# Optimization experiments

Measured on AMD Instinct MI355X. Metric: run time of the kernel, lower is better.

## Reference

```python
import jax, jax.numpy as jnp
import numpy as np

WIDTH = 64
HEIGHT = 64
FEAT = 128
LAT = 64
NUM_SLOTS = 7


def pixel_coords(img_size):
    g = jnp.linspace(-1.0, 1.0, img_size)
    g1, g2 = jnp.meshgrid(g, g, indexing='ij')  # matches torch.meshgrid default
    return jnp.stack([g1, g2], axis=0)[None]  # (1, 2, S, S)


def clamp_pg(x, lo, hi):
    # clamp that preserves gradients (straight-through)
    return x + jax.lax.stop_gradient(jnp.clip(x, lo, hi) - x)


def setup_inputs() -> dict:
    key = jax.random.key(0)
    k0, k1, k2, k3 = jax.random.split(key, 4)
    bs = 64
    x = jax.random.normal(k0, (bs, FEAT, WIDTH, HEIGHT), jnp.float32)
    rand_pixel = jax.random.uniform(k1, (bs, 1, WIDTH, HEIGHT), jnp.float32)
    conv_w = jax.random.normal(k2, (LAT, FEAT), jnp.float32) / np.sqrt(FEAT)
    conv_b = jax.random.normal(k3, (LAT,), jnp.float32) * 0.01
    gate = jnp.asarray(0.5, jnp.float32)  # ScalarGate parameter (nonzero so c_f is non-degenerate)
    # laplacian kernel: sigma_init = 1 / (sqrt(num_slots) * log 2)
    log_sigma = jnp.asarray(np.log(1.0 / (np.sqrt(NUM_SLOTS) * np.log(2.0))), jnp.float32)
    return {'x': x, 'rand_pixel': rand_pixel, 'conv_w': conv_w, 'conv_b': conv_b,
            'gate': gate, 'log_sigma': log_sigma, 'num_cl_steps': 6}


def _forward(x, rand_pixel, conv_w, conv_b, gate, log_sigma, num_cl_steps):
    bs = x.shape[0]
    # SemiConv: gated 1x1 conv + fixed uv coordinate channels
    out = gate * (jnp.einsum('of,bfhw->bohw', conv_w, x) + conv_b[None, :, None, None])
    uv = jnp.concatenate([jnp.zeros((1, LAT - 2, WIDTH, HEIGHT), out.dtype),
                          pixel_coords(WIDTH).astype(out.dtype)], axis=1)
    c_f = out + uv                      # (bs, LAT, W, H)
    delta = out[:, -2:]                 # (bs, 2, W, H)
    sigma = jnp.exp(log_sigma)
    c_flat = c_f.reshape(bs, LAT, -1)   # (bs, LAT, W*H)
    b_idx = jnp.arange(bs)
    log_s0 = jnp.zeros((bs, 1, WIDTH, HEIGHT), c_f.dtype)

    def step(log_s, _):
        # interpolate-to-same-size is identity -> scope = exp(log_s)
        probs = (rand_pixel * jnp.exp(log_s)).reshape(bs, -1)
        idx = jnp.argmax(probs, axis=1)                 # (bs,)
        seed = c_flat[b_idx, :, idx]                    # (bs, LAT)
        diff = c_f - seed[:, :, None, None]
        dist = jnp.sqrt(clamp_pg((diff ** 2).sum(1), 1e-10, 1e10))  # euclidian (laplacian kernel)
        alpha = jnp.exp(-dist / sigma)[:, None]         # (bs, 1, W, H)
        alpha = clamp_pg(alpha, 0.01, 0.99)
        log_m = log_s + jnp.log(alpha)
        new_log_s = log_s + jnp.log1p(-alpha)
        return new_log_s, (log_m, new_log_s, seed)

    log_s_final, (log_m_steps, log_s_steps, seeds) = jax.lax.scan(
        step, log_s0, None, length=num_cl_steps)
    # log_m_k has num_cl_steps masks plus the final scope appended
    log_m_k = jnp.concatenate([log_m_steps, log_s_final[None]], axis=0)
    log_s_k = jnp.concatenate([log_s0[None], log_s_steps], axis=0)
    return log_m_k, log_s_k, c_f, delta, seeds


def reference(x, rand_pixel, conv_w, conv_b, gate, log_sigma, num_cl_steps):
    return _forward(x, rand_pixel, conv_w, conv_b, gate, log_sigma, num_cl_steps)
```

## Files before the change

kernel.cpp:

```cpp
#include <hip/hip_runtime.h>
#include <hip/hip_bf16.h>

#define NPIX 4096
#define FEAT 128
#define LAT 64
#define BS 64
#define NSTEPS 6

#define OFF_LOGM  0u
#define OFF_LOGS  1835008u
#define OFF_CF    3670016u
#define OFF_DELTA 20447232u
#define OFF_SEEDS 20971520u

typedef float f32x4 __attribute__((ext_vector_type(4)));
typedef short s16x8 __attribute__((ext_vector_type(8)));

__device__ __forceinline__ void amax_comb(float& bv, int& bi, float v, int i) {
    if (v > bv || (v == bv && i < bi)) { bv = v; bi = i; }
}

__device__ __forceinline__ short f2bf_rne(float r) {
    __hip_bfloat16 h = __float2bfloat16(r);
    return __builtin_bit_cast(short, h);
}

__device__ __forceinline__ void split2(float v, short& hi, short& lo) {
    unsigned u = __builtin_bit_cast(unsigned, v);
    hi = (short)(u >> 16);
    float hf = __builtin_bit_cast(float, u & 0xFFFF0000u);
    lo = f2bf_rne(v - hf);
}

__device__ __forceinline__ void transpose4(float4& v, int b) {
    float4 w;
    w.x = __shfl_xor(v.x, 1, 64); w.y = __shfl_xor(v.y, 1, 64);
    w.z = __shfl_xor(v.z, 1, 64); w.w = __shfl_xor(v.w, 1, 64);
    float4 u;
    if ((b & 1) == 0) u = make_float4(v.x, w.x, v.z, w.z);
    else              u = make_float4(w.y, v.y, w.w, v.w);
    float4 w2;
    w2.x = __shfl_xor(u.x, 2, 64); w2.y = __shfl_xor(u.y, 2, 64);
    w2.z = __shfl_xor(u.z, 2, 64); w2.w = __shfl_xor(u.w, 2, 64);
    if ((b & 2) == 0) v = make_float4(u.x, u.y, w2.x, w2.y);
    else              v = make_float4(w2.z, w2.w, u.z, u.w);
}

__global__ void prep_w(const float* __restrict__ w, const float* __restrict__ gate_p,
                       short* __restrict__ gwh, short* __restrict__ gwl)
{
    int i = blockIdx.x * 256 + threadIdx.x;
    float v = gate_p[0] * w[i];
    short h, l; split2(v, h, l);
    gwh[i] = h; gwl[i] = l;
}

__global__ __launch_bounds__(512, 4) void conv_mfma(
    const float* __restrict__ x, const float* __restrict__ rand_pixel,
    const float* __restrict__ bias, const float* __restrict__ gate_p,
    float* __restrict__ out,
    float* __restrict__ pval, int* __restrict__ pidx, int* __restrict__ cnt,
    const short* __restrict__ gwh, const short* __restrict__ gwl)
{
    __shared__ __align__(16) short Xhi[256][40];
    __shared__ __align__(16) short Xlo[256][40];
    __shared__ __align__(16) short Whi[64][132];
    __shared__ __align__(16) short Wlo[64][132];
    __shared__ float sbias[64];

    const int tid  = threadIdx.x;
    const int b    = blockIdx.x >> 4;
    const int tile = blockIdx.x & 15;
    const int p0   = tile * 256;
    const int lane = tid & 63;
    const int wv   = tid >> 6;
    const int l15  = lane & 15;
    const int lg   = lane >> 4;
    const int oh   = wv >> 2;
    const int pxq  = wv & 3;

    const int q  = tid >> 2;
    const int j  = tid & 3;
    const int P  = (q & 63) * 4;
    const int g0 = q >> 6;

    if (tile == 0 && tid < 8) cnt[b * 8 + tid] = 0;
    if (tid < 64) sbias[tid] = gate_p[0] * bias[tid];

    {
        const int o = tid >> 3, c = (tid & 7) * 16;
        *(s16x8*)&Whi[o][c]     = *(const s16x8*)&gwh[o * 128 + c];
        *(s16x8*)&Whi[o][c + 8] = *(const s16x8*)&gwh[o * 128 + c + 8];
        *(s16x8*)&Wlo[o][c]     = *(const s16x8*)&gwl[o * 128 + c];
        *(s16x8*)&Wlo[o][c + 8] = *(const s16x8*)&gwl[o * 128 + c + 8];
    }

    const float* xb = x + (size_t)b * FEAT * NPIX + p0;
    float4 v[4];
    #pragma unroll
    for (int i = 0; i < 4; ++i) {
        int g = g0 + 2 * i;
        v[i] = *(const float4*)(xb + (size_t)(g * 4 + j) * NPIX + P);
    }
    #pragma unroll
    for (int i = 0; i < 4; ++i) {
        int g = g0 + 2 * i;
        float4 t = v[i]; transpose4(t, j);
        short h0, l0, h1, l1, h2, l2, h3, l3;
        split2(t.x, h0, l0); split2(t.y, h1, l1);
        split2(t.z, h2, l2); split2(t.w, h3, l3);
        *(short4*)&Xhi[P + j][g * 4] = make_short4(h0, h1, h2, h3);
        *(short4*)&Xlo[P + j][g * 4] = make_short4(l0, l1, l2, l3);
    }
    __syncthreads();

    f32x4 acc[2][4];
    #pragma unroll
    for (int og2 = 0; og2 < 2; ++og2)
        #pragma unroll
        for (int pg = 0; pg < 4; ++pg)
            acc[og2][pg] = (f32x4){0.f, 0.f, 0.f, 0.f};

    #pragma unroll
    for (int kc = 0; kc < 4; ++kc) {
        if (kc < 3) {
            #pragma unroll
            for (int i = 0; i < 4; ++i) {
                int g = g0 + 2 * i;
                v[i] = *(const float4*)(xb + (size_t)((kc + 1) * 32 + g * 4 + j) * NPIX + P);
            }
        }

        s16x8 Ah[2], Al[2];
        #pragma unroll
        for (int og2 = 0; og2 < 2; ++og2) {
            int o = oh * 32 + og2 * 16 + l15;
            Ah[og2] = *(const s16x8*)&Whi[o][kc * 32 + lg * 8];
            Al[og2] = *(const s16x8*)&Wlo[o][kc * 32 + lg * 8];
        }

        #pragma unroll
        for (int pg = 0; pg < 4; ++pg) {
            int pxl = pxq * 64 + pg * 16 + l15;
            s16x8 Bh = *(const s16x8*)&Xhi[pxl][lg * 8];
            s16x8 Bl = *(const s16x8*)&Xlo[pxl][lg * 8];
            #pragma unroll
            for (int og2 = 0; og2 < 2; ++og2) {
                acc[og2][pg] = __builtin_amdgcn_mfma_f32_16x16x32_bf16(Ah[og2], Bh, acc[og2][pg], 0, 0, 0);
                acc[og2][pg] = __builtin_amdgcn_mfma_f32_16x16x32_bf16(Ah[og2], Bl, acc[og2][pg], 0, 0, 0);
                acc[og2][pg] = __builtin_amdgcn_mfma_f32_16x16x32_bf16(Al[og2], Bh, acc[og2][pg], 0, 0, 0);
            }
        }

        if (kc < 3) {
            __syncthreads();
            #pragma unroll
            for (int i = 0; i < 4; ++i) {
                int g = g0 + 2 * i;
                float4 t = v[i]; transpose4(t, j);
                short h0, l0, h1, l1, h2, l2, h3, l3;
                split2(t.x, h0, l0); split2(t.y, h1, l1);
                split2(t.z, h2, l2); split2(t.w, h3, l3);
                *(short4*)&Xhi[P + j][g * 4] = make_short4(h0, h1, h2, h3);
                *(short4*)&Xlo[P + j][g * 4] = make_short4(l0, l1, l2, l3);
            }
            __syncthreads();
        }
    }

    float* cf = out + OFF_CF + (size_t)b * LAT * NPIX;
    #pragma unroll
    for (int og2 = 0; og2 < 2; ++og2) {
        #pragma unroll
        for (int pg = 0; pg < 4; ++pg) {
            #pragma unroll
            for (int r = 0; r < 4; ++r) {
                int o = oh * 32 + og2 * 16 + lg * 4 + r;
                int p = p0 + pxq * 64 + pg * 16 + l15;
                float vv = acc[og2][pg][r] + sbias[o];
                if (o == 62) {
                    out[OFF_DELTA + ((size_t)b * 2 + 0) * NPIX + p] = vv;
                    vv += (float)(-1.0 + 2.0 * (double)(p >> 6) / 63.0);
                } else if (o == 63) {
                    out[OFF_DELTA + ((size_t)b * 2 + 1) * NPIX + p] = vv;
                    vv += (float)(-1.0 + 2.0 * (double)(p & 63) / 63.0);
                }
                cf[(size_t)o * NPIX + p] = vv;
            }
        }
    }

    if (wv == 0) {
        *(float4*)(out + OFF_LOGS + (size_t)b * NPIX + p0 + lane * 4) =
            make_float4(0.f, 0.f, 0.f, 0.f);
        float4 rv = *(const float4*)(rand_pixel + (size_t)b * NPIX + p0 + lane * 4);
        int pb = p0 + lane * 4;
        float bv = rv.x; int bi = pb;
        if (rv.y > bv) { bv = rv.y; bi = pb + 1; }
        if (rv.z > bv) { bv = rv.z; bi = pb + 2; }
        if (rv.w > bv) { bv = rv.w; bi = pb + 3; }
        #pragma unroll
        for (int off = 32; off > 0; off >>= 1) {
            float ov = __shfl_down(bv, off, 64);
            int   oi = __shfl_down(bi, off, 64);
            amax_comb(bv, bi, ov, oi);
        }
        if (lane == 0) { pval[blockIdx.x] = bv; pidx[blockIdx.x] = bi; }
    }
}

#define REP16(OP) OP(0) OP(1) OP(2) OP(3) OP(4) OP(5) OP(6) OP(7) \
                  OP(8) OP(9) OP(10) OP(11) OP(12) OP(13) OP(14) OP(15)

__global__ __launch_bounds__(1024, 4) void steps_fused(
    const float* __restrict__ rand_pixel, const float* __restrict__ log_sigma_p,
    float* __restrict__ out, float* pv, int* pi, int* cnt)
{
    __shared__ float s_mv[16];
    __shared__ int   s_mi[16];
    __shared__ __align__(16) float s_seed[LAT];
    __shared__ float s_rv[16];
    __shared__ int   s_ri[16];

    const int tid  = threadIdx.x;
    const int b    = blockIdx.x & 63;
    const int tile = blockIdx.x >> 6;
    const int p    = tile * 1024 + tid;

    const float* cfb = out + OFF_CF + (size_t)b * LAT * NPIX;

#define AG_DECL(i) float ag##i##_0, ag##i##_1, ag##i##_2, ag##i##_3;
    REP16(AG_DECL)
#define AG_PARK(i) { \
    float v0 = cfb[(size_t)(4*i+0)*NPIX + p]; \
    float v1 = cfb[(size_t)(4*i+1)*NPIX + p]; \
    float v2 = cfb[(size_t)(4*i+2)*NPIX + p]; \
    float v3 = cfb[(size_t)(4*i+3)*NPIX + p]; \
    asm volatile("v_accvgpr_write_b32 %0, %1" : "=a"(ag##i##_0) : "v"(v0)); \
    asm volatile("v_accvgpr_write_b32 %0, %1" : "=a"(ag##i##_1) : "v"(v1)); \
    asm volatile("v_accvgpr_write_b32 %0, %1" : "=a"(ag##i##_2) : "v"(v2)); \
    asm volatile("v_accvgpr_write_b32 %0, %1" : "=a"(ag##i##_3) : "v"(v3)); }
    REP16(AG_PARK)

    const float rp    = rand_pixel[(size_t)b * NPIX + p];
    const float sigma = expf(log_sigma_p[0]);
    float ls = 0.f;

    #pragma unroll 1
    for (int s = 0; s < NSTEPS; ++s) {
        if (s > 0) {
            if (tid == 0) {
                while (__hip_atomic_load(&cnt[b * 8 + s], __ATOMIC_ACQUIRE,
                                         __HIP_MEMORY_SCOPE_AGENT) < 4)
                    __builtin_amdgcn_s_sleep(2);
            }
            __syncthreads();
        }
        const int nmerge = (s == 0) ? 16 : 4;
        if (tid < nmerge) {
            s_mv[tid] = __hip_atomic_load(&pv[(s * BS + b) * 16 + tid],
                                          __ATOMIC_RELAXED, __HIP_MEMORY_SCOPE_AGENT);
            s_mi[tid] = __hip_atomic_load(&pi[(s * BS + b) * 16 + tid],
                                          __ATOMIC_RELAXED, __HIP_MEMORY_SCOPE_AGENT);
        }
        __syncthreads();

        float bv = -1.0f; int bi = 0;
        for (int k = 0; k < nmerge; ++k) amax_comb(bv, bi, s_mv[k], s_mi[k]);

        if (tid < LAT) s_seed[tid] = cfb[(size_t)tid * NPIX + bi];
        __syncthreads();
        if (tile == 0 && tid < LAT)
            out[OFF_SEEDS + ((size_t)s * BS + b) * LAT + tid] = s_seed[tid];

        float d2 = 0.f;
#define AG_DIFF(i) { \
        float c0, c1, c2, c3; \
        asm volatile("v_accvgpr_read_b32 %0, %1" : "=v"(c0) : "a"(ag##i##_0)); \
        asm volatile("v_accvgpr_read_b32 %0, %1" : "=v"(c1) : "a"(ag##i##_1)); \
        asm volatile("v_accvgpr_read_b32 %0, %1" : "=v"(c2) : "a"(ag##i##_2)); \
        asm volatile("v_accvgpr_read_b32 %0, %1" : "=v"(c3) : "a"(ag##i##_3)); \
        float e0 = c0 - s_seed[4*i+0]; d2 = fmaf(e0, e0, d2); \
        float e1 = c1 - s_seed[4*i+1]; d2 = fmaf(e1, e1, d2); \
        float e2 = c2 - s_seed[4*i+2]; d2 = fmaf(e2, e2, d2); \
        float e3 = c3 - s_seed[4*i+3]; d2 = fmaf(e3, e3, d2); }
        REP16(AG_DIFF)

        float dist  = sqrtf(fminf(fmaxf(d2, 1e-10f), 1e10f));
        float alpha = expf(-dist / sigma);
        alpha = fminf(fmaxf(alpha, 0.01f), 0.99f);
        float lm  = ls + logf(alpha);
        float lsn = ls + log1pf(-alpha);

        out[OFF_LOGM + ((size_t)s * BS + b) * NPIX + p]       = lm;
        out[OFF_LOGS + ((size_t)(s + 1) * BS + b) * NPIX + p] = lsn;
        ls = lsn;

        if (s == NSTEPS - 1) {
            out[OFF_LOGM + ((size_t)NSTEPS * BS + b) * NPIX + p] = lsn;
        } else {
            float prob = rp * expf(lsn);
            int   idx  = p;
            #pragma unroll
            for (int off = 32; off > 0; off >>= 1) {
                float ov = __shfl_down(prob, off, 64);
                int   oi = __shfl_down(idx, off, 64);
                amax_comb(prob, idx, ov, oi);
            }
            int lane = tid & 63, wid = tid >> 6;
            if (lane == 0) { s_rv[wid] = prob; s_ri[wid] = idx; }
            __syncthreads();
            if (tid == 0) {
                float fb = s_rv[0]; int fi = s_ri[0];
                #pragma unroll
                for (int k = 1; k < 16; ++k) amax_comb(fb, fi, s_rv[k], s_ri[k]);
                __hip_atomic_store(&pv[((s + 1) * BS + b) * 16 + tile], fb,
                                   __ATOMIC_RELAXED, __HIP_MEMORY_SCOPE_AGENT);
                __hip_atomic_store(&pi[((s + 1) * BS + b) * 16 + tile], fi,
                                   __ATOMIC_RELAXED, __HIP_MEMORY_SCOPE_AGENT);
                __hip_atomic_fetch_add(&cnt[b * 8 + s + 1], 1,
                                       __ATOMIC_RELEASE, __HIP_MEMORY_SCOPE_AGENT);
            }
        }
    }
}

__global__ __launch_bounds__(1024, 4) void step_kernel(
    const float* __restrict__ rand_pixel, const float* __restrict__ log_sigma_p,
    float* __restrict__ out, float* pv, int* pi, int step)
{
    __shared__ float s_mv[16];
    __shared__ int   s_mi[16];
    __shared__ __align__(16) float s_seed[LAT];
    __shared__ float s_rv[16];
    __shared__ int   s_ri[16];

    const int tid  = threadIdx.x;
    const int b    = blockIdx.x & 63;
    const int tile = blockIdx.x >> 6;
    const int p    = tile * 1024 + tid;

    const float* cfb = out + OFF_CF + (size_t)b * LAT * NPIX;

    const int nmerge = (step == 0) ? 16 : 4;
    if (tid < nmerge) { s_mv[tid] = pv[(step * BS + b) * 16 + tid];
                        s_mi[tid] = pi[(step * BS + b) * 16 + tid]; }
    __syncthreads();
    float bv = -1.0f; int bi = 0;
    for (int k = 0; k < nmerge; ++k) amax_comb(bv, bi, s_mv[k], s_mi[k]);

    if (tid < LAT) s_seed[tid] = cfb[(size_t)tid * NPIX + bi];
    __syncthreads();
    if (tile == 0 && tid < LAT)
        out[OFF_SEEDS + ((size_t)step * BS + b) * LAT + tid] = s_seed[tid];

    float d2 = 0.f;
    #pragma unroll
    for (int c = 0; c < LAT; ++c) {
        float d = cfb[(size_t)c * NPIX + p] - s_seed[c];
        d2 = fmaf(d, d, d2);
    }
    float dist  = sqrtf(fminf(fmaxf(d2, 1e-10f), 1e10f));
    float sigma = expf(log_sigma_p[0]);
    float alpha = expf(-dist / sigma);
    alpha = fminf(fmaxf(alpha, 0.01f), 0.99f);

    float ls  = out[OFF_LOGS + ((size_t)step * BS + b) * NPIX + p];
    float lm  = ls + logf(alpha);
    float lsn = ls + log1pf(-alpha);

    out[OFF_LOGM + ((size_t)step * BS + b) * NPIX + p]       = lm;
    out[OFF_LOGS + ((size_t)(step + 1) * BS + b) * NPIX + p] = lsn;
    if (step == NSTEPS - 1)
        out[OFF_LOGM + ((size_t)NSTEPS * BS + b) * NPIX + p] = lsn;

    if (step < NSTEPS - 1) {
        float prob = rand_pixel[(size_t)b * NPIX + p] * expf(lsn);
        int   idx  = p;
        #pragma unroll
        for (int off = 32; off > 0; off >>= 1) {
            float ov = __shfl_down(prob, off, 64);
            int   oi = __shfl_down(idx, off, 64);
            amax_comb(prob, idx, ov, oi);
        }
        int lane = tid & 63, wid = tid >> 6;
        if (lane == 0) { s_rv[wid] = prob; s_ri[wid] = idx; }
        __syncthreads();
        if (tid == 0) {
            float fb = s_rv[0]; int fi = s_ri[0];
            #pragma unroll
            for (int k = 1; k < 16; ++k) amax_comb(fb, fi, s_rv[k], s_ri[k]);
            pv[((step + 1) * BS + b) * 16 + tile] = fb;
            pi[((step + 1) * BS + b) * 16 + tile] = fi;
        }
    }
}

extern "C" void kernel_launch(void* const* d_in, const int* in_sizes, int n_in,
                              void* d_out, int out_size, void* d_ws, size_t ws_size,
                              hipStream_t stream) {
    const float* x          = (const float*)d_in[0];
    const float* rand_pixel = (const float*)d_in[1];
    const float* w          = (const float*)d_in[2];
    const float* bias       = (const float*)d_in[3];
    const float* gate       = (const float*)d_in[4];
    const float* log_sigma  = (const float*)d_in[5];

    float* out = (float*)d_out;
    float* pv  = (float*)d_ws;
    int*   pi  = (int*)((char*)d_ws + 24576);
    int*   cnt = (int*)((char*)d_ws + 49152);
    short* gwh = (short*)((char*)d_ws + 51200);
    short* gwl = (short*)((char*)d_ws + 67584);

    prep_w<<<32, 256, 0, stream>>>(w, gate, gwh, gwl);
    conv_mfma<<<1024, 512, 0, stream>>>(x, rand_pixel, bias, gate, out,
                                        pv, pi, cnt, gwh, gwl);

    const float* a0 = rand_pixel; const float* a1 = log_sigma; float* a2 = out;
    float* a3 = pv; int* a4 = pi; int* a5 = cnt;
    void* kp[6] = {(void*)&a0, (void*)&a1, (void*)&a2, (void*)&a3, (void*)&a4, (void*)&a5};
    hipError_t e = hipLaunchCooperativeKernel((const void*)steps_fused,
                                              dim3(256), dim3(1024), kp, 0, stream);
    if (e != hipSuccess) {
        for (int s = 0; s < NSTEPS; ++s)
            step_kernel<<<256, 1024, 0, stream>>>(rand_pixel, log_sigma, out, pv, pi, s);
    }
}
```

Baseline: 124.7 us.

## Merge conv and clustering steps into one cooperative kernel with per-batch flags

```diff
diff --git a/kernel.cpp b/kernel.cpp
--- a/kernel.cpp
+++ b/kernel.cpp
@@ -47,19 +47,24 @@
 }
 
 __global__ void prep_w(const float* __restrict__ w, const float* __restrict__ gate_p,
-                       short* __restrict__ gwh, short* __restrict__ gwl)
+                       short* __restrict__ gwh, short* __restrict__ gwl,
+                       int* __restrict__ cnt)
 {
     int i = blockIdx.x * 256 + threadIdx.x;
     float v = gate_p[0] * w[i];
     short h, l; split2(v, h, l);
     gwh[i] = h; gwl[i] = l;
-}
-
-__global__ __launch_bounds__(512, 4) void conv_mfma(
+    if (i < BS * 8) cnt[i] = 0;
+}
+
+#define REP16(OP) OP(0) OP(1) OP(2) OP(3) OP(4) OP(5) OP(6) OP(7) \
+                  OP(8) OP(9) OP(10) OP(11) OP(12) OP(13) OP(14) OP(15)
+
+__global__ __launch_bounds__(512, 4) void merged(
     const float* __restrict__ x, const float* __restrict__ rand_pixel,
     const float* __restrict__ bias, const float* __restrict__ gate_p,
-    float* __restrict__ out,
-    float* __restrict__ pval, int* __restrict__ pidx, int* __restrict__ cnt,
+    const float* __restrict__ log_sigma_p, float* __restrict__ out,
+    float* pv, int* pi, int* cnt,
     const short* __restrict__ gwh, const short* __restrict__ gwl)
 {
     __shared__ __align__(16) short Xhi[256][40];
@@ -67,11 +72,17 @@
     __shared__ __align__(16) short Whi[64][132];
     __shared__ __align__(16) short Wlo[64][132];
     __shared__ float sbias[64];
+    __shared__ float s_pv[2];
+    __shared__ int   s_pi[2];
+    __shared__ float s_mv[8];
+    __shared__ int   s_mi[8];
+    __shared__ __align__(16) float s_seed[LAT];
+    __shared__ float s_rv[8];
+    __shared__ int   s_ri[8];
 
     const int tid  = threadIdx.x;
-    const int b    = blockIdx.x >> 4;
-    const int tile = blockIdx.x & 15;
-    const int p0   = tile * 256;
+    const int b    = blockIdx.x >> 3;
+    const int t8   = blockIdx.x & 7;
     const int lane = tid & 63;
     const int wv   = tid >> 6;
     const int l15  = lane & 15;
@@ -84,7 +95,6 @@
     const int P  = (q & 63) * 4;
     const int g0 = q >> 6;
 
-    if (tile == 0 && tid < 8) cnt[b * 8 + tid] = 0;
     if (tid < 64) sbias[tid] = gate_p[0] * bias[tid];
 
     {
@@ -95,142 +105,159 @@
         *(s16x8*)&Wlo[o][c + 8] = *(const s16x8*)&gwl[o * 128 + c + 8];
     }
 
-    const float* xb = x + (size_t)b * FEAT * NPIX + p0;
-    float4 v[4];
-    #pragma unroll
-    for (int i = 0; i < 4; ++i) {
-        int g = g0 + 2 * i;
-        v[i] = *(const float4*)(xb + (size_t)(g * 4 + j) * NPIX + P);
-    }
-    #pragma unroll
-    for (int i = 0; i < 4; ++i) {
-        int g = g0 + 2 * i;
-        float4 t = v[i]; transpose4(t, j);
-        short h0, l0, h1, l1, h2, l2, h3, l3;
-        split2(t.x, h0, l0); split2(t.y, h1, l1);
-        split2(t.z, h2, l2); split2(t.w, h3, l3);
-        *(short4*)&Xhi[P + j][g * 4] = make_short4(h0, h1, h2, h3);
-        *(short4*)&Xlo[P + j][g * 4] = make_short4(l0, l1, l2, l3);
-    }
+    #pragma unroll 1
+    for (int half = 0; half < 2; ++half) {
+        const int tile = t8 * 2 + half;
+        const int p0   = tile * 256;
+        const float* xb = x + (size_t)b * FEAT * NPIX + p0;
+
+        __syncthreads();
+
+        float4 v[4];
+        #pragma unroll
+        for (int i = 0; i < 4; ++i) {
+            int g = g0 + 2 * i;
+            v[i] = *(const float4*)(xb + (size_t)(g * 4 + j) * NPIX + P);
+        }
+        #pragma unroll
+        for (int i = 0; i < 4; ++i) {
+            int g = g0 + 2 * i;
+            float4 t = v[i]; transpose4(t, j);
+            short h0, l0, h1, l1, h2, l2, h3, l3;
+            split2(t.x, h0, l0); split2(t.y, h1, l1);
+            split2(t.z, h2, l2); split2(t.w, h3, l3);
+            *(short4*)&Xhi[P + j][g * 4] = make_short4(h0, h1, h2, h3);
+            *(short4*)&Xlo[P + j][g * 4] = make_short4(l0, l1, l2, l3);
+        }
+        __syncthreads();
+
+        f32x4 acc[2][4];
+        #pragma unroll
+        for (int og2 = 0; og2 < 2; ++og2)
+            #pragma unroll
+            for (int pg = 0; pg < 4; ++pg)
+                acc[og2][pg] = (f32x4){0.f, 0.f, 0.f, 0.f};
+
+        #pragma unroll
+        for (int kc = 0; kc < 4; ++kc) {
+            if (kc < 3) {
+                #pragma unroll
+                for (int i = 0; i < 4; ++i) {
+                    int g = g0 + 2 * i;
+                    v[i] = *(const float4*)(xb + (size_t)((kc + 1) * 32 + g * 4 + j) * NPIX + P);
+                }
+            }
+
+            s16x8 Ah[2], Al[2];
+            #pragma unroll
+            for (int og2 = 0; og2 < 2; ++og2) {
+                int o = oh * 32 + og2 * 16 + l15;
+                Ah[og2] = *(const s16x8*)&Whi[o][kc * 32 + lg * 8];
+                Al[og2] = *(const s16x8*)&Wlo[o][kc * 32 + lg * 8];
+            }
+
+            #pragma unroll
+            for (int pg = 0; pg < 4; ++pg) {
+                int pxl = pxq * 64 + pg * 16 + l15;
+                s16x8 Bh = *(const s16x8*)&Xhi[pxl][lg * 8];
+                s16x8 Bl = *(const s16x8*)&Xlo[pxl][lg * 8];
+                #pragma unroll
+                for (int og2 = 0; og2 < 2; ++og2) {
+                    acc[og2][pg] = __builtin_amdgcn_mfma_f32_16x16x32_bf16(Ah[og2], Bh, acc[og2][pg], 0, 0, 0);
+                    acc[og2][pg] = __builtin_amdgcn_mfma_f32_16x16x32_bf16(Ah[og2], Bl, acc[og2][pg], 0, 0, 0);
+                    acc[og2][pg] = __builtin_amdgcn_mfma_f32_16x16x32_bf16(Al[og2], Bh, acc[og2][pg], 0, 0, 0);
+                }
+            }
+
+            if (kc < 3) {
+                __syncthreads();
+                #pragma unroll
+                for (int i = 0; i < 4; ++i) {
+                    int g = g0 + 2 * i;
+                    float4 t = v[i]; transpose4(t, j);
+                    short h0, l0, h1, l1, h2, l2, h3, l3;
+                    split2(t.x, h0, l0); split2(t.y, h1, l1);
+                    split2(t.z, h2, l2); split2(t.w, h3, l3);
+                    *(short4*)&Xhi[P + j][g * 4] = make_short4(h0, h1, h2, h3);
+                    *(short4*)&Xlo[P + j][g * 4] = make_short4(l0, l1, l2, l3);
+                }
+                __syncthreads();
+            }
+        }
+
+        float* cf = out + OFF_CF + (size_t)b * LAT * NPIX;
+        #pragma unroll
+        for (int og2 = 0; og2 < 2; ++og2) {
+            #pragma unroll
+            for (int pg = 0; pg < 4; ++pg) {
+                #pragma unroll
+                for (int r = 0; r < 4; ++r) {
+                    int o = oh * 32 + og2 * 16 + lg * 4 + r;
+                    int p = p0 + pxq * 64 + pg * 16 + l15;
+                    float vv = acc[og2][pg][r] + sbias[o];
+                    if (o == 62) {
+                        out[OFF_DELTA + ((size_t)b * 2 + 0) * NPIX + p] = vv;
+                        vv += (float)(-1.0 + 2.0 * (double)(p >> 6) / 63.0);
+                    } else if (o == 63) {
+                        out[OFF_DELTA + ((size_t)b * 2 + 1) * NPIX + p] = vv;
+                        vv += (float)(-1.0 + 2.0 * (double)(p & 63) / 63.0);
+                    }
+                    cf[(size_t)o * NPIX + p] = vv;
+                }
+            }
+        }
+
+        if (wv == 0) {
+            *(float4*)(out + OFF_LOGS + (size_t)b * NPIX + p0 + lane * 4) =
+                make_float4(0.f, 0.f, 0.f, 0.f);
+            float4 rv = *(const float4*)(rand_pixel + (size_t)b * NPIX + p0 + lane * 4);
+            int pb = p0 + lane * 4;
+            float bv = rv.x; int bi = pb;
+            if (rv.y > bv) { bv = rv.y; bi = pb + 1; }
+            if (rv.z > bv) { bv = rv.z; bi = pb + 2; }
+            if (rv.w > bv) { bv = rv.w; bi = pb + 3; }
+            #pragma unroll
+            for (int off = 32; off > 0; off >>= 1) {
+                float ov = __shfl_down(bv, off, 64);
+                int   oi = __shfl_down(bi, off, 64);
+                amax_comb(bv, bi, ov, oi);
+            }
+            if (lane == 0) { s_pv[half] = bv; s_pi[half] = bi; }
+        }
+    }
+
     __syncthreads();
-
-    f32x4 acc[2][4];
-    #pragma unroll
-    for (int og2 = 0; og2 < 2; ++og2)
-        #pragma unroll
-        for (int pg = 0; pg < 4; ++pg)
-            acc[og2][pg] = (f32x4){0.f, 0.f, 0.f, 0.f};
-
-    #pragma unroll
-    for (int kc = 0; kc < 4; ++kc) {
-        if (kc < 3) {
-            #pragma unroll
-            for (int i = 0; i < 4; ++i) {
-                int g = g0 + 2 * i;
-                v[i] = *(const float4*)(xb + (size_t)((kc + 1) * 32 + g * 4 + j) * NPIX + P);
-            }
-        }
-
-        s16x8 Ah[2], Al[2];
-        #pragma unroll
-        for (int og2 = 0; og2 < 2; ++og2) {
-            int o = oh * 32 + og2 * 16 + l15;
-            Ah[og2] = *(const s16x8*)&Whi[o][kc * 32 + lg * 8];
-            Al[og2] = *(const s16x8*)&Wlo[o][kc * 32 + lg * 8];
-        }
-
-        #pragma unroll
-        for (int pg = 0; pg < 4; ++pg) {
-            int pxl = pxq * 64 + pg * 16 + l15;
-            s16x8 Bh = *(const s16x8*)&Xhi[pxl][lg * 8];
-            s16x8 Bl = *(const s16x8*)&Xlo[pxl][lg * 8];
-            #pragma unroll
-            for (int og2 = 0; og2 < 2; ++og2) {
-                acc[og2][pg] = __builtin_amdgcn_mfma_f32_16x16x32_bf16(Ah[og2], Bh, acc[og2][pg], 0, 0, 0);
-                acc[og2][pg] = __builtin_amdgcn_mfma_f32_16x16x32_bf16(Ah[og2], Bl, acc[og2][pg], 0, 0, 0);
-                acc[og2][pg] = __builtin_amdgcn_mfma_f32_16x16x32_bf16(Al[og2], Bh, acc[og2][pg], 0, 0, 0);
-            }
-        }
-
-        if (kc < 3) {
-            __syncthreads();
-            #pragma unroll
-            for (int i = 0; i < 4; ++i) {
-                int g = g0 + 2 * i;
-                float4 t = v[i]; transpose4(t, j);
-                short h0, l0, h1, l1, h2, l2, h3, l3;
-                split2(t.x, h0, l0); split2(t.y, h1, l1);
-                split2(t.z, h2, l2); split2(t.w, h3, l3);
-                *(short4*)&Xhi[P + j][g * 4] = make_short4(h0, h1, h2, h3);
-                *(short4*)&Xlo[P + j][g * 4] = make_short4(l0, l1, l2, l3);
-            }
-            __syncthreads();
-        }
-    }
-
-    float* cf = out + OFF_CF + (size_t)b * LAT * NPIX;
-    #pragma unroll
-    for (int og2 = 0; og2 < 2; ++og2) {
-        #pragma unroll
-        for (int pg = 0; pg < 4; ++pg) {
-            #pragma unroll
-            for (int r = 0; r < 4; ++r) {
-                int o = oh * 32 + og2 * 16 + lg * 4 + r;
-                int p = p0 + pxq * 64 + pg * 16 + l15;
-                float vv = acc[og2][pg][r] + sbias[o];
-                if (o == 62) {
-                    out[OFF_DELTA + ((size_t)b * 2 + 0) * NPIX + p] = vv;
-                    vv += (float)(-1.0 + 2.0 * (double)(p >> 6) / 63.0);
-                } else if (o == 63) {
-                    out[OFF_DELTA + ((size_t)b * 2 + 1) * NPIX + p] = vv;
-                    vv += (float)(-1.0 + 2.0 * (double)(p & 63) / 63.0);
-                }
-                cf[(size_t)o * NPIX + p] = vv;
-            }
-        }
-    }
-
-    if (wv == 0) {
-        *(float4*)(out + OFF_LOGS + (size_t)b * NPIX + p0 + lane * 4) =
-            make_float4(0.f, 0.f, 0.f, 0.f);
-        float4 rv = *(const float4*)(rand_pixel + (size_t)b * NPIX + p0 + lane * 4);
-        int pb = p0 + lane * 4;
-        float bv = rv.x; int bi = pb;
-        if (rv.y > bv) { bv = rv.y; bi = pb + 1; }
-        if (rv.z > bv) { bv = rv.z; bi = pb + 2; }
-        if (rv.w > bv) { bv = rv.w; bi = pb + 3; }
-        #pragma unroll
-        for (int off = 32; off > 0; off >>= 1) {
-            float ov = __shfl_down(bv, off, 64);
-            int   oi = __shfl_down(bi, off, 64);
-            amax_comb(bv, bi, ov, oi);
-        }
-        if (lane == 0) { pval[blockIdx.x] = bv; pidx[blockIdx.x] = bi; }
-    }
-}
-
-#define REP16(OP) OP(0) OP(1) OP(2) OP(3) OP(4) OP(5) OP(6) OP(7) \
-                  OP(8) OP(9) OP(10) OP(11) OP(12) OP(13) OP(14) OP(15)
-
-__global__ __launch_bounds__(1024, 4) void steps_fused(
-    const float* __restrict__ rand_pixel, const float* __restrict__ log_sigma_p,
-    float* __restrict__ out, float* pv, int* pi, int* cnt)
-{
-    __shared__ float s_mv[16];
-    __shared__ int   s_mi[16];
-    __shared__ __align__(16) float s_seed[LAT];
-    __shared__ float s_rv[16];
-    __shared__ int   s_ri[16];
-
-    const int tid  = threadIdx.x;
-    const int b    = blockIdx.x & 63;
-    const int tile = blockIdx.x >> 6;
-    const int p    = tile * 1024 + tid;
-
+    if (tid == 0) {
+        float fb = s_pv[0]; int fi = s_pi[0];
+        amax_comb(fb, fi, s_pv[1], s_pi[1]);
+        __hip_atomic_store(&pv[(0 * BS + b) * 8 + t8], fb,
+                           __ATOMIC_RELAXED, __HIP_MEMORY_SCOPE_AGENT);
+        __hip_atomic_store(&pi[(0 * BS + b) * 8 + t8], fi,
+                           __ATOMIC_RELAXED, __HIP_MEMORY_SCOPE_AGENT);
+        __hip_atomic_fetch_add(&cnt[b * 8 + 0], 1,
+                               __ATOMIC_RELEASE, __HIP_MEMORY_SCOPE_AGENT);
+    }
+
+    const int p = t8 * 512 + tid;
     const float* cfb = out + OFF_CF + (size_t)b * LAT * NPIX;
 
 #define AG_DECL(i) float ag##i##_0, ag##i##_1, ag##i##_2, ag##i##_3;
     REP16(AG_DECL)
+
+    const float rp    = rand_pixel[(size_t)b * NPIX + p];
+    const float sigma = expf(log_sigma_p[0]);
+    float ls = 0.f;
+
+    #pragma unroll 1
+    for (int s = 0; s < NSTEPS; ++s) {
+        if (tid == 0) {
+            while (__hip_atomic_load(&cnt[b * 8 + s], __ATOMIC_ACQUIRE,
+                                     __HIP_MEMORY_SCOPE_AGENT) < 8)
+                __builtin_amdgcn_s_sleep(2);
+        }
+        __syncthreads();
+
+        if (s == 0) {
 #define AG_PARK(i) { \
     float v0 = cfb[(size_t)(4*i+0)*NPIX + p]; \
     float v1 = cfb[(size_t)(4*i+1)*NPIX + p]; \
@@ -240,37 +267,24 @@
     asm volatile("v_accvgpr_write_b32 %0, %1" : "=a"(ag##i##_1) : "v"(v1)); \
     asm volatile("v_accvgpr_write_b32 %0, %1" : "=a"(ag##i##_2) : "v"(v2)); \
     asm volatile("v_accvgpr_write_b32 %0, %1" : "=a"(ag##i##_3) : "v"(v3)); }
-    REP16(AG_PARK)
-
-    const float rp    = rand_pixel[(size_t)b * NPIX + p];
-    const float sigma = expf(log_sigma_p[0]);
-    float ls = 0.f;
-
-    #pragma unroll 1
-    for (int s = 0; s < NSTEPS; ++s) {
-        if (s > 0) {
-            if (tid == 0) {
-                while (__hip_atomic_load(&cnt[b * 8 + s], __ATOMIC_ACQUIRE,
-                                         __HIP_MEMORY_SCOPE_AGENT) < 4)
-                    __builtin_amdgcn_s_sleep(2);
-            }
-            __syncthreads();
-        }
-        const int nmerge = (s == 0) ? 16 : 4;
-        if (tid < nmerge) {
-            s_mv[tid] = __hip_atomic_load(&pv[(s * BS + b) * 16 + tid],
+            REP16(AG_PARK)
+        }
+
+        if (tid < 8) {
+            s_mv[tid] = __hip_atomic_load(&pv[(s * BS + b) * 8 + tid],
                                           __ATOMIC_RELAXED, __HIP_MEMORY_SCOPE_AGENT);
-            s_mi[tid] = __hip_atomic_load(&pi[(s * BS + b) * 16 + tid],
+            s_mi[tid] = __hip_atomic_load(&pi[(s * BS + b) * 8 + tid],
                                           __ATOMIC_RELAXED, __HIP_MEMORY_SCOPE_AGENT);
         }
         __syncthreads();
 
         float bv = -1.0f; int bi = 0;
-        for (int k = 0; k < nmerge; ++k) amax_comb(bv, bi, s_mv[k], s_mi[k]);
+        #pragma unroll
+        for (int k = 0; k < 8; ++k) amax_comb(bv, bi, s_mv[k], s_mi[k]);
 
         if (tid < LAT) s_seed[tid] = cfb[(size_t)tid * NPIX + bi];
         __syncthreads();
-        if (tile == 0 && tid < LAT)
+        if (t8 == 0 && tid < LAT)
             out[OFF_SEEDS + ((size_t)s * BS + b) * LAT + tid] = s_seed[tid];
 
         float d2 = 0.f;
@@ -307,91 +321,19 @@
                 int   oi = __shfl_down(idx, off, 64);
                 amax_comb(prob, idx, ov, oi);
             }
-            int lane = tid & 63, wid = tid >> 6;
-            if (lane == 0) { s_rv[wid] = prob; s_ri[wid] = idx; }
+            if (lane == 0) { s_rv[wv] = prob; s_ri[wv] = idx; }
             __syncthreads();
             if (tid == 0) {
                 float fb = s_rv[0]; int fi = s_ri[0];
                 #pragma unroll
-                for (int k = 1; k < 16; ++k) amax_comb(fb, fi, s_rv[k], s_ri[k]);
-                __hip_atomic_store(&pv[((s + 1) * BS + b) * 16 + tile], fb,
+                for (int k = 1; k < 8; ++k) amax_comb(fb, fi, s_rv[k], s_ri[k]);
+                __hip_atomic_store(&pv[((s + 1) * BS + b) * 8 + t8], fb,
                                    __ATOMIC_RELAXED, __HIP_MEMORY_SCOPE_AGENT);
-                __hip_atomic_store(&pi[((s + 1) * BS + b) * 16 + tile], fi,
+                __hip_atomic_store(&pi[((s + 1) * BS + b) * 8 + t8], fi,
                                    __ATOMIC_RELAXED, __HIP_MEMORY_SCOPE_AGENT);
                 __hip_atomic_fetch_add(&cnt[b * 8 + s + 1], 1,
                                        __ATOMIC_RELEASE, __HIP_MEMORY_SCOPE_AGENT);
             }
-        }
-    }
-}
-
-__global__ __launch_bounds__(1024, 4) void step_kernel(
-    const float* __restrict__ rand_pixel, const float* __restrict__ log_sigma_p,
-    float* __restrict__ out, float* pv, int* pi, int step)
-{
-    __shared__ float s_mv[16];
-    __shared__ int   s_mi[16];
-    __shared__ __align__(16) float s_seed[LAT];
-    __shared__ float s_rv[16];
-    __shared__ int   s_ri[16];
-
-    const int tid  = threadIdx.x;
-    const int b    = blockIdx.x & 63;
-    const int tile = blockIdx.x >> 6;
-    const int p    = tile * 1024 + tid;
-
-    const float* cfb = out + OFF_CF + (size_t)b * LAT * NPIX;
-
-    const int nmerge = (step == 0) ? 16 : 4;
-    if (tid < nmerge) { s_mv[tid] = pv[(step * BS + b) * 16 + tid];
-                        s_mi[tid] = pi[(step * BS + b) * 16 + tid]; }
-    __syncthreads();
-    float bv = -1.0f; int bi = 0;
-    for (int k = 0; k < nmerge; ++k) amax_comb(bv, bi, s_mv[k], s_mi[k]);
-
-    if (tid < LAT) s_seed[tid] = cfb[(size_t)tid * NPIX + bi];
-    __syncthreads();
-    if (tile == 0 && tid < LAT)
-        out[OFF_SEEDS + ((size_t)step * BS + b) * LAT + tid] = s_seed[tid];
-
-    float d2 = 0.f;
-    #pragma unroll
-    for (int c = 0; c < LAT; ++c) {
-        float d = cfb[(size_t)c * NPIX + p] - s_seed[c];
-        d2 = fmaf(d, d, d2);
-    }
-    float dist  = sqrtf(fminf(fmaxf(d2, 1e-10f), 1e10f));
-    float sigma = expf(log_sigma_p[0]);
-    float alpha = expf(-dist / sigma);
-    alpha = fminf(fmaxf(alpha, 0.01f), 0.99f);
-
-    float ls  = out[OFF_LOGS + ((size_t)step * BS + b) * NPIX + p];
-    float lm  = ls + logf(alpha);
-    float lsn = ls + log1pf(-alpha);
-
-    out[OFF_LOGM + ((size_t)step * BS + b) * NPIX + p]       = lm;
-    out[OFF_LOGS + ((size_t)(step + 1) * BS + b) * NPIX + p] = lsn;
-    if (step == NSTEPS - 1)
-        out[OFF_LOGM + ((size_t)NSTEPS * BS + b) * NPIX + p] = lsn;
-
-    if (step < NSTEPS - 1) {
-        float prob = rand_pixel[(size_t)b * NPIX + p] * expf(lsn);
-        int   idx  = p;
-        #pragma unroll
-        for (int off = 32; off > 0; off >>= 1) {
-            float ov = __shfl_down(prob, off, 64);
-            int   oi = __shfl_down(idx, off, 64);
-            amax_comb(prob, idx, ov, oi);
-        }
-        int lane = tid & 63, wid = tid >> 6;
-        if (lane == 0) { s_rv[wid] = prob; s_ri[wid] = idx; }
-        __syncthreads();
-        if (tid == 0) {
-            float fb = s_rv[0]; int fi = s_ri[0];
-            #pragma unroll
-            for (int k = 1; k < 16; ++k) amax_comb(fb, fi, s_rv[k], s_ri[k]);
-            pv[((step + 1) * BS + b) * 16 + tile] = fb;
-            pi[((step + 1) * BS + b) * 16 + tile] = fi;
         }
     }
 }
@@ -408,22 +350,24 @@
 
     float* out = (float*)d_out;
     float* pv  = (float*)d_ws;
-    int*   pi  = (int*)((char*)d_ws + 24576);
-    int*   cnt = (int*)((char*)d_ws + 49152);
-    short* gwh = (short*)((char*)d_ws + 51200);
-    short* gwl = (short*)((char*)d_ws + 67584);
-
-    prep_w<<<32, 256, 0, stream>>>(w, gate, gwh, gwl);
-    conv_mfma<<<1024, 512, 0, stream>>>(x, rand_pixel, bias, gate, out,
-                                        pv, pi, cnt, gwh, gwl);
-
-    const float* a0 = rand_pixel; const float* a1 = log_sigma; float* a2 = out;
-    float* a3 = pv; int* a4 = pi; int* a5 = cnt;
-    void* kp[6] = {(void*)&a0, (void*)&a1, (void*)&a2, (void*)&a3, (void*)&a4, (void*)&a5};
-    hipError_t e = hipLaunchCooperativeKernel((const void*)steps_fused,
-                                              dim3(256), dim3(1024), kp, 0, stream);
+    int*   pi  = (int*)((char*)d_ws + 12288);
+    int*   cnt = (int*)((char*)d_ws + 24576);
+    short* gwh = (short*)((char*)d_ws + 26624);
+    short* gwl = (short*)((char*)d_ws + 43008);
+
+    prep_w<<<32, 256, 0, stream>>>(w, gate, gwh, gwl, cnt);
+
+    const float* a0 = x; const float* a1 = rand_pixel; const float* a2 = bias;
+    const float* a3 = gate; const float* a4 = log_sigma; float* a5 = out;
+    float* a6 = pv; int* a7 = pi; int* a8 = cnt;
+    const short* a9 = gwh; const short* a10 = gwl;
+    void* kp[11] = {(void*)&a0, (void*)&a1, (void*)&a2, (void*)&a3, (void*)&a4,
+                    (void*)&a5, (void*)&a6, (void*)&a7, (void*)&a8, (void*)&a9,
+                    (void*)&a10};
+    hipError_t e = hipLaunchCooperativeKernel((const void*)merged,
+                                              dim3(512), dim3(512), kp, 0, stream);
     if (e != hipSuccess) {
-        for (int s = 0; s < NSTEPS; ++s)
-            step_kernel<<<256, 1024, 0, stream>>>(rand_pixel, log_sigma, out, pv, pi, s);
-    }
-}
+        merged<<<512, 512, 0, stream>>>(x, rand_pixel, bias, gate, log_sigma,
+                                        out, pv, pi, cnt, gwh, gwl);
+    }
+}
```

New measurement: 254.3 us. 104% more time.

## Keep conv weight fragments in AGPRs instead of LDS and raise occupancy

Applied to the files above, without the earlier changes.

```diff
diff --git a/kernel.cpp b/kernel.cpp
--- a/kernel.cpp
+++ b/kernel.cpp
@@ -46,6 +46,9 @@
     else              v = make_float4(w2.z, w2.w, u.z, u.w);
 }
 
+#define AWR(d, s) asm volatile("v_accvgpr_write_b32 %0, %1" : "=a"(d) : "v"(s));
+#define ARD(d, s) asm volatile("v_accvgpr_read_b32 %0, %1" : "=v"(d) : "a"(s));
+
 __global__ void prep_w(const float* __restrict__ w, const float* __restrict__ gate_p,
                        short* __restrict__ gwh, short* __restrict__ gwl)
 {
@@ -55,7 +58,75 @@
     gwh[i] = h; gwl[i] = l;
 }
 
-__global__ __launch_bounds__(512, 4) void conv_mfma(
+
+#define WFRAG_DECL(kc) \
+    float wh_##kc##_0_0, wh_##kc##_0_1, wh_##kc##_0_2, wh_##kc##_0_3; \
+    float wh_##kc##_1_0, wh_##kc##_1_1, wh_##kc##_1_2, wh_##kc##_1_3; \
+    float wl_##kc##_0_0, wl_##kc##_0_1, wl_##kc##_0_2, wl_##kc##_0_3; \
+    float wl_##kc##_1_0, wl_##kc##_1_1, wl_##kc##_1_2, wl_##kc##_1_3;
+
+#define WFRAG_PARK(kc) { \
+    uint4 h0 = *(const uint4*)&gwh[(oh * 32 + 0 * 16 + l15) * 128 + kc * 32 + lg * 8]; \
+    uint4 h1 = *(const uint4*)&gwh[(oh * 32 + 1 * 16 + l15) * 128 + kc * 32 + lg * 8]; \
+    uint4 l0 = *(const uint4*)&gwl[(oh * 32 + 0 * 16 + l15) * 128 + kc * 32 + lg * 8]; \
+    uint4 l1 = *(const uint4*)&gwl[(oh * 32 + 1 * 16 + l15) * 128 + kc * 32 + lg * 8]; \
+    AWR(wh_##kc##_0_0, h0.x) AWR(wh_##kc##_0_1, h0.y) AWR(wh_##kc##_0_2, h0.z) AWR(wh_##kc##_0_3, h0.w) \
+    AWR(wh_##kc##_1_0, h1.x) AWR(wh_##kc##_1_1, h1.y) AWR(wh_##kc##_1_2, h1.z) AWR(wh_##kc##_1_3, h1.w) \
+    AWR(wl_##kc##_0_0, l0.x) AWR(wl_##kc##_0_1, l0.y) AWR(wl_##kc##_0_2, l0.z) AWR(wl_##kc##_0_3, l0.w) \
+    AWR(wl_##kc##_1_0, l1.x) AWR(wl_##kc##_1_1, l1.y) AWR(wl_##kc##_1_2, l1.z) AWR(wl_##kc##_1_3, l1.w) }
+
+#define WFRAG_UNPARK(kc, Ah, Al) { \
+    unsigned u0, u1, u2, u3; uint4 uu; \
+    ARD(u0, wh_##kc##_0_0) ARD(u1, wh_##kc##_0_1) ARD(u2, wh_##kc##_0_2) ARD(u3, wh_##kc##_0_3) \
+    uu = make_uint4(u0, u1, u2, u3); Ah[0] = __builtin_bit_cast(s16x8, uu); \
+    ARD(u0, wh_##kc##_1_0) ARD(u1, wh_##kc##_1_1) ARD(u2, wh_##kc##_1_2) ARD(u3, wh_##kc##_1_3) \
+    uu = make_uint4(u0, u1, u2, u3); Ah[1] = __builtin_bit_cast(s16x8, uu); \
+    ARD(u0, wl_##kc##_0_0) ARD(u1, wl_##kc##_0_1) ARD(u2, wl_##kc##_0_2) ARD(u3, wl_##kc##_0_3) \
+    uu = make_uint4(u0, u1, u2, u3); Al[0] = __builtin_bit_cast(s16x8, uu); \
+    ARD(u0, wl_##kc##_1_0) ARD(u1, wl_##kc##_1_1) ARD(u2, wl_##kc##_1_2) ARD(u3, wl_##kc##_1_3) \
+    uu = make_uint4(u0, u1, u2, u3); Al[1] = __builtin_bit_cast(s16x8, uu); }
+
+#define STAGE_WRITE() { \
+    _Pragma("unroll") \
+    for (int i = 0; i < 4; ++i) { \
+        int g = g0 + 2 * i; \
+        float4 t = v[i]; transpose4(t, j); \
+        short h0, l0, h1, l1, h2, l2, h3, l3; \
+        split2(t.x, h0, l0); split2(t.y, h1, l1); \
+        split2(t.z, h2, l2); split2(t.w, h3, l3); \
+        *(short4*)&Xhi[P + j][g * 4] = make_short4(h0, h1, h2, h3); \
+        *(short4*)&Xlo[P + j][g * 4] = make_short4(l0, l1, l2, l3); \
+    } }
+
+#define CHUNK(kc) { \
+    if (kc < 3) { \
+        _Pragma("unroll") \
+        for (int i = 0; i < 4; ++i) { \
+            int g = g0 + 2 * i; \
+            v[i] = *(const float4*)(xb + (size_t)((kc + 1) * 32 + g * 4 + j) * NPIX + P); \
+        } \
+    } \
+    s16x8 Ah[2], Al[2]; \
+    WFRAG_UNPARK(kc, Ah, Al) \
+    _Pragma("unroll") \
+    for (int pg = 0; pg < 4; ++pg) { \
+        int pxl = pxq * 64 + pg * 16 + l15; \
+        s16x8 Bh = *(const s16x8*)&Xhi[pxl][lg * 8]; \
+        s16x8 Bl = *(const s16x8*)&Xlo[pxl][lg * 8]; \
+        _Pragma("unroll") \
+        for (int og2 = 0; og2 < 2; ++og2) { \
+            acc[og2][pg] = __builtin_amdgcn_mfma_f32_16x16x32_bf16(Ah[og2], Bh, acc[og2][pg], 0, 0, 0); \
+            acc[og2][pg] = __builtin_amdgcn_mfma_f32_16x16x32_bf16(Ah[og2], Bl, acc[og2][pg], 0, 0, 0); \
+            acc[og2][pg] = __builtin_amdgcn_mfma_f32_16x16x32_bf16(Al[og2], Bh, acc[og2][pg], 0, 0, 0); \
+        } \
+    } \
+    if (kc < 3) { \
+        __syncthreads(); \
+        STAGE_WRITE() \
+        __syncthreads(); \
+    } }
+
+__global__ __launch_bounds__(512, 6) void conv_mfma(
     const float* __restrict__ x, const float* __restrict__ rand_pixel,
     const float* __restrict__ bias, const float* __restrict__ gate_p,
     float* __restrict__ out,
@@ -64,8 +135,6 @@
 {
     __shared__ __align__(16) short Xhi[256][40];
     __shared__ __align__(16) short Xlo[256][40];
-    __shared__ __align__(16) short Whi[64][132];
-    __shared__ __align__(16) short Wlo[64][132];
     __shared__ float sbias[64];
 
     const int tid  = threadIdx.x;
@@ -87,13 +156,8 @@
     if (tile == 0 && tid < 8) cnt[b * 8 + tid] = 0;
     if (tid < 64) sbias[tid] = gate_p[0] * bias[tid];
 
-    {
-        const int o = tid >> 3, c = (tid & 7) * 16;
-        *(s16x8*)&Whi[o][c]     = *(const s16x8*)&gwh[o * 128 + c];
-        *(s16x8*)&Whi[o][c + 8] = *(const s16x8*)&gwh[o * 128 + c + 8];
-        *(s16x8*)&Wlo[o][c]     = *(const s16x8*)&gwl[o * 128 + c];
-        *(s16x8*)&Wlo[o][c + 8] = *(const s16x8*)&gwl[o * 128 + c + 8];
-    }
+    WFRAG_DECL(0) WFRAG_DECL(1) WFRAG_DECL(2) WFRAG_DECL(3)
+    WFRAG_PARK(0) WFRAG_PARK(1) WFRAG_PARK(2) WFRAG_PARK(3)
 
     const float* xb = x + (size_t)b * FEAT * NPIX + p0;
     float4 v[4];
@@ -102,16 +166,7 @@
         int g = g0 + 2 * i;
         v[i] = *(const float4*)(xb + (size_t)(g * 4 + j) * NPIX + P);
     }
-    #pragma unroll
-    for (int i = 0; i < 4; ++i) {
-        int g = g0 + 2 * i;
-        float4 t = v[i]; transpose4(t, j);
-        short h0, l0, h1, l1, h2, l2, h3, l3;
-        split2(t.x, h0, l0); split2(t.y, h1, l1);
-        split2(t.z, h2, l2); split2(t.w, h3, l3);
-        *(short4*)&Xhi[P + j][g * 4] = make_short4(h0, h1, h2, h3);
-        *(short4*)&Xlo[P + j][g * 4] = make_short4(l0, l1, l2, l3);
-    }
+    STAGE_WRITE()
     __syncthreads();
 
     f32x4 acc[2][4];
@@ -121,52 +176,7 @@
         for (int pg = 0; pg < 4; ++pg)
             acc[og2][pg] = (f32x4){0.f, 0.f, 0.f, 0.f};
 
-    #pragma unroll
-    for (int kc = 0; kc < 4; ++kc) {
-        if (kc < 3) {
-            #pragma unroll
-            for (int i = 0; i < 4; ++i) {
-                int g = g0 + 2 * i;
-                v[i] = *(const float4*)(xb + (size_t)((kc + 1) * 32 + g * 4 + j) * NPIX + P);
-            }
-        }
-
-        s16x8 Ah[2], Al[2];
-        #pragma unroll
-        for (int og2 = 0; og2 < 2; ++og2) {
-            int o = oh * 32 + og2 * 16 + l15;
-            Ah[og2] = *(const s16x8*)&Whi[o][kc * 32 + lg * 8];
-            Al[og2] = *(const s16x8*)&Wlo[o][kc * 32 + lg * 8];
-        }
-
-        #pragma unroll
-        for (int pg = 0; pg < 4; ++pg) {
-            int pxl = pxq * 64 + pg * 16 + l15;
-            s16x8 Bh = *(const s16x8*)&Xhi[pxl][lg * 8];
-            s16x8 Bl = *(const s16x8*)&Xlo[pxl][lg * 8];
-            #pragma unroll
-            for (int og2 = 0; og2 < 2; ++og2) {
-                acc[og2][pg] = __builtin_amdgcn_mfma_f32_16x16x32_bf16(Ah[og2], Bh, acc[og2][pg], 0, 0, 0);
-                acc[og2][pg] = __builtin_amdgcn_mfma_f32_16x16x32_bf16(Ah[og2], Bl, acc[og2][pg], 0, 0, 0);
-                acc[og2][pg] = __builtin_amdgcn_mfma_f32_16x16x32_bf16(Al[og2], Bh, acc[og2][pg], 0, 0, 0);
-            }
-        }
-
-        if (kc < 3) {
-            __syncthreads();
-            #pragma unroll
-            for (int i = 0; i < 4; ++i) {
-                int g = g0 + 2 * i;
-                float4 t = v[i]; transpose4(t, j);
-                short h0, l0, h1, l1, h2, l2, h3, l3;
-                split2(t.x, h0, l0); split2(t.y, h1, l1);
-                split2(t.z, h2, l2); split2(t.w, h3, l3);
-                *(short4*)&Xhi[P + j][g * 4] = make_short4(h0, h1, h2, h3);
-                *(short4*)&Xlo[P + j][g * 4] = make_short4(l0, l1, l2, l3);
-            }
-            __syncthreads();
-        }
-    }
+    CHUNK(0) CHUNK(1) CHUNK(2) CHUNK(3)
 
     float* cf = out + OFF_CF + (size_t)b * LAT * NPIX;
     #pragma unroll
@@ -236,10 +246,7 @@
     float v1 = cfb[(size_t)(4*i+1)*NPIX + p]; \
     float v2 = cfb[(size_t)(4*i+2)*NPIX + p]; \
     float v3 = cfb[(size_t)(4*i+3)*NPIX + p]; \
-    asm volatile("v_accvgpr_write_b32 %0, %1" : "=a"(ag##i##_0) : "v"(v0)); \
-    asm volatile("v_accvgpr_write_b32 %0, %1" : "=a"(ag##i##_1) : "v"(v1)); \
-    asm volatile("v_accvgpr_write_b32 %0, %1" : "=a"(ag##i##_2) : "v"(v2)); \
-    asm volatile("v_accvgpr_write_b32 %0, %1" : "=a"(ag##i##_3) : "v"(v3)); }
+    AWR(ag##i##_0, v0) AWR(ag##i##_1, v1) AWR(ag##i##_2, v2) AWR(ag##i##_3, v3) }
     REP16(AG_PARK)
 
     const float rp    = rand_pixel[(size_t)b * NPIX + p];
@@ -276,10 +283,7 @@
         float d2 = 0.f;
 #define AG_DIFF(i) { \
         float c0, c1, c2, c3; \
-        asm volatile("v_accvgpr_read_b32 %0, %1" : "=v"(c0) : "a"(ag##i##_0)); \
-        asm volatile("v_accvgpr_read_b32 %0, %1" : "=v"(c1) : "a"(ag##i##_1)); \
-        asm volatile("v_accvgpr_read_b32 %0, %1" : "=v"(c2) : "a"(ag##i##_2)); \
-        asm volatile("v_accvgpr_read_b32 %0, %1" : "=v"(c3) : "a"(ag##i##_3)); \
+        ARD(c0, ag##i##_0) ARD(c1, ag##i##_1) ARD(c2, ag##i##_2) ARD(c3, ag##i##_3) \
         float e0 = c0 - s_seed[4*i+0]; d2 = fmaf(e0, e0, d2); \
         float e1 = c1 - s_seed[4*i+1]; d2 = fmaf(e1, e1, d2); \
         float e2 = c2 - s_seed[4*i+2]; d2 = fmaf(e2, e2, d2); \
```

After: 196.9 us. +57.9%, slower.
